# Kernel tuning notes

Hardware: AMD Instinct MI355X
Metric: run time of the kernel (lower is better)

## Reference

```python
import jax, jax.numpy as jnp
import numpy as np

N_NODES = 10000
N_EDGES = 640000
HID = 128


def setup_inputs() -> dict:
    key = jax.random.key(0)
    ks = jax.random.split(key, 8)
    h = jax.random.normal(ks[0], (N_NODES, HID), dtype=jnp.float32)
    edge_index = jax.random.randint(ks[1], (2, N_EDGES), 0, N_NODES, dtype=jnp.int64)
    edge_attr = jax.random.normal(ks[2], (N_EDGES, 1), dtype=jnp.float32)
    s1 = 1.0 / np.sqrt(2 * HID + 1)
    s2 = 1.0 / np.sqrt(HID)
    s3 = 1.0 / np.sqrt(2 * HID)
    return {
        "h": h,
        "edge_index": edge_index,
        "edge_attr": edge_attr,
        "msg_w1": jax.random.normal(ks[3], (2 * HID + 1, HID), dtype=jnp.float32) * s1,
        "msg_b1": jnp.zeros((HID,), dtype=jnp.float32),
        "msg_w2": jax.random.normal(ks[4], (HID, HID), dtype=jnp.float32) * s2,
        "msg_b2": jnp.zeros((HID,), dtype=jnp.float32),
        "upd_w1": jax.random.normal(ks[5], (2 * HID, HID), dtype=jnp.float32) * s3,
        "upd_b1": jnp.zeros((HID,), dtype=jnp.float32),
        "upd_w2": jax.random.normal(ks[6], (HID, HID), dtype=jnp.float32) * s2,
        "upd_b2": jnp.zeros((HID,), dtype=jnp.float32),
    }


def reference(h, edge_index, edge_attr, msg_w1, msg_b1, msg_w2, msg_b2,
              upd_w1, upd_b1, upd_w2, upd_b2):
    src, dst = edge_index[0], edge_index[1]
    # gather -> concat: [E, 2*HID+1]
    m_in = jnp.concatenate([h[src], h[dst], edge_attr], axis=1)
    # message MLP
    msg = jax.nn.relu(m_in @ msg_w1 + msg_b1) @ msg_w2 + msg_b2
    # scatter-add over destination nodes: [N, HID]
    agg = jax.ops.segment_sum(msg, dst, num_segments=h.shape[0])
    # update MLP with residual
    upd_in = jnp.concatenate([h, agg], axis=1)
    upd = jax.nn.relu(upd_in @ upd_w1 + upd_b1) @ upd_w2 + upd_b2
    return h + upd
```

## Files before the change

kernel.cpp:

```cpp
#include <hip/hip_runtime.h>
#include <hip/hip_bf16.h>

#define HID 128
#define NNODES 10000
#define NEDGES 640000
#define NBIN 625
#define NPB 16
#define BINCAP 1408
#define SCATB 250
#define EPT 10
#define SLAB 2560
#define PBOS 640

typedef __attribute__((ext_vector_type(8))) short bf16x8;
typedef __attribute__((ext_vector_type(4))) float f32x4;

__device__ inline short f2bf(float f) {
  unsigned u = __builtin_bit_cast(unsigned, f);
  u = (u + 0x7fffu + ((u >> 16) & 1u)) >> 16;
  return (short)u;
}
__device__ inline float bf2f(unsigned short u) {
  unsigned ui = ((unsigned)u) << 16;
  return __builtin_bit_cast(float, ui);
}

__global__ __launch_bounds__(256) void k_partA(
    const int* __restrict__ eidxraw, const float* __restrict__ ea,
    uint2* __restrict__ part, int* __restrict__ pbo,
    const float* __restrict__ h,
    const float* __restrict__ mw1, const float* __restrict__ mw2,
    const float* __restrict__ uw1, const float* __restrict__ uw2,
    short* __restrict__ pW2, short* __restrict__ pU1, short* __restrict__ pU2,
    const float* __restrict__ b1,
    short* __restrict__ Xs, short* __restrict__ cvecbf) {
  __shared__ int histL[NBIN + 1];
  __shared__ int offsL[NBIN + 1];
  __shared__ int spL[256];
  __shared__ __align__(16) uint2 slab[SLAB];
  const int bid = blockIdx.x;
  const int tid = threadIdx.x;

  if (bid < SCATB) {
    for (int i = tid; i < NBIN + 1; i += 256) histL[i] = 0;
    __syncthreads();
    bool is64 = true;
#pragma unroll
    for (int k = 0; k < 16; ++k) is64 = is64 && (eidxraw[2 * k + 1] == 0);
    unsigned pk[EPT];
    float av[EPT];
    const int ebase = bid * SLAB;
#pragma unroll
    for (int r = 0; r < EPT; ++r) {
      int e = ebase + r * 256 + tid;
      int sv = is64 ? eidxraw[2 * e] : eidxraw[e];
      int dv = is64 ? eidxraw[2 * (NEDGES + e)] : eidxraw[NEDGES + e];
      pk[r] = ((unsigned)dv << 16) | (unsigned)sv;
      av[r] = ea[e];
      atomicAdd(&histL[dv >> 4], 1);
    }
    __syncthreads();
    int c0 = 0, c1 = 0, c2 = 0;
    {
      int b0 = tid * 3;
      if (b0 < NBIN) c0 = histL[b0];
      if (b0 + 1 < NBIN) c1 = histL[b0 + 1];
      if (b0 + 2 < NBIN) c2 = histL[b0 + 2];
    }
    int s = c0 + c1 + c2;
    spL[tid] = s;
    __syncthreads();
    for (int d = 1; d < 256; d <<= 1) {
      int v = (tid >= d) ? spL[tid - d] : 0;
      __syncthreads();
      spL[tid] += v;
      __syncthreads();
    }
    int run = spL[tid] - s;
    {
      int b0 = tid * 3;
      if (b0 < NBIN)     { offsL[b0] = run;     histL[b0] = run;     run += c0; }
      if (b0 + 1 < NBIN) { offsL[b0 + 1] = run; histL[b0 + 1] = run; run += c1; }
      if (b0 + 2 < NBIN) { offsL[b0 + 2] = run; histL[b0 + 2] = run; }
    }
    if (tid == 255) offsL[NBIN] = spL[255];
    __syncthreads();
#pragma unroll
    for (int r = 0; r < EPT; ++r) {
      int bin = pk[r] >> 20;
      int pos = atomicAdd(&histL[bin], 1);
      slab[pos] = make_uint2(pk[r], __builtin_bit_cast(unsigned, av[r]));
    }
    __syncthreads();
    for (int i = tid; i < SLAB; i += 256) part[bid * SLAB + i] = slab[i];
    for (int i = tid; i < NBIN + 1; i += 256) pbo[bid * PBOS + i] = offsL[i];
  } else if (bid < 282) {
    int pb = bid - SCATB;
    const float* W; short* outp; int t;
    if (pb < 8)       { W = mw2; outp = pW2; t = pb * 256; }
    else if (pb < 24) { W = uw1; outp = pU1; t = (pb - 8) * 256; }
    else              { W = uw2; outp = pU2; t = (pb - 24) * 256; }
    t += tid;
    int ll = t & 63, nt = (t >> 6) & 7, kt = t >> 9;
    int col = nt * 16 + (ll & 15);
    int k0 = kt * 32 + ((ll >> 4) << 3);
    bf16x8 o;
#pragma unroll
    for (int j = 0; j < 8; ++j) o[j] = f2bf(W[(k0 + j) * HID + col]);
    reinterpret_cast<bf16x8*>(outp)[t] = o;
  } else {
    const int wv = tid >> 6, l = tid & 63;
    const int lr = l & 15, lg = l >> 4;
    const int rbase = (bid - 282) * 64 + wv * 16;
    int rA = rbase + lr;
    if (rA > NNODES - 1) rA = NNODES - 1;
    const float* hrow = h + (size_t)rA * HID;
    const float* W1a = mw1;
    const float* W1b = mw1 + 128 * HID;

    const f32x4 zero = {0.f, 0.f, 0.f, 0.f};
    f32x4 accA[8], accB[8];
#pragma unroll
    for (int nt = 0; nt < 8; ++nt) { accA[nt] = zero; accB[nt] = zero; }
#pragma unroll
    for (int kt = 0; kt < 4; ++kt) {
      f32x4 a0 = *reinterpret_cast<const f32x4*>(hrow + kt * 32 + lg * 8);
      f32x4 a1 = *reinterpret_cast<const f32x4*>(hrow + kt * 32 + lg * 8 + 4);
      bf16x8 af;
#pragma unroll
      for (int j = 0; j < 4; ++j) { af[j] = f2bf(a0[j]); af[4 + j] = f2bf(a1[j]); }
      const int k0 = kt * 32 + lg * 8;
#pragma unroll
      for (int nt = 0; nt < 8; ++nt) {
        const int col = nt * 16 + lr;
        bf16x8 bfa, bfb;
#pragma unroll
        for (int j = 0; j < 8; ++j) {
          bfa[j] = f2bf(W1a[(k0 + j) * HID + col]);
          bfb[j] = f2bf(W1b[(k0 + j) * HID + col]);
        }
        accA[nt] = __builtin_amdgcn_mfma_f32_16x16x32_bf16(af, bfa, accA[nt], 0, 0, 0);
        accB[nt] = __builtin_amdgcn_mfma_f32_16x16x32_bf16(af, bfb, accB[nt], 0, 0, 0);
      }
    }
#pragma unroll
    for (int nt = 0; nt < 8; ++nt) {
      const int col = nt * 16 + lr;
      const float bb = b1[col];
#pragma unroll
      for (int i = 0; i < 4; ++i) {
        int row = rbase + lg * 4 + i;
        if (row < NNODES) {
          ((unsigned short*)Xs)[row * HID + col] = (unsigned short)f2bf(accA[nt][i]);
          ((unsigned short*)cvecbf)[row * HID + col] = (unsigned short)f2bf(accB[nt][i] + bb);
        }
      }
    }
  }
}

__global__ __launch_bounds__(256) void k_merged(
    const short* __restrict__ Xs, const uint2* __restrict__ part,
    const int* __restrict__ pbo, const short* __restrict__ cvecbf,
    const float* __restrict__ w1raw, const float* __restrict__ hf,
    const short* __restrict__ pW2, const float* __restrict__ b2,
    const short* __restrict__ pU1, const float* __restrict__ bu1,
    const short* __restrict__ pU2, const float* __restrict__ bu2,
    float* __restrict__ out) {
  __shared__ __align__(16) uint2 eraw[BINCAP];
  __shared__ __align__(16) uint2 efin[BINCAP];
  __shared__ __align__(16) short ldsR[NPB][136];
  __shared__ int spL[256];
  __shared__ int cnt16[NPB], off16[NPB], cur16[NPB];
  short* ldsA = (short*)eraw;
  short* ldsB = (short*)efin;
  const int b = blockIdx.x;
  const int tid = threadIdx.x;
  const int wv = tid >> 6, l = tid & 63;
  const int lr = l & 15, lg = l >> 4;
  const int nb = b * NPB;

  if (tid < NPB) cnt16[tid] = 0;
  int o0 = 0, cnt_t = 0;
  if (tid < SCATB) {
    o0 = pbo[tid * PBOS + b];
    cnt_t = pbo[tid * PBOS + b + 1] - o0;
  }
  spL[tid] = cnt_t;
  __syncthreads();
  for (int d = 1; d < 256; d <<= 1) {
    int v = (tid >= d) ? spL[tid - d] : 0;
    __syncthreads();
    spL[tid] += v;
    __syncthreads();
  }
  const int base = spL[tid] - cnt_t;
  for (int i = 0; i < cnt_t; ++i) {
    uint2 ent = part[tid * SLAB + o0 + i];
    int pos = base + i;
    if (pos < BINCAP) {
      atomicAdd(&cnt16[(int)(ent.x >> 16) & 15], 1);
      eraw[pos] = ent;
    }
  }
  __syncthreads();
  int total = spL[255];
  if (total > BINCAP) total = BINCAP;
  if (tid < NPB) {
    int v = cnt16[tid];
    int x = v;
#pragma unroll
    for (int d = 1; d < NPB; d <<= 1) {
      int y = __shfl_up(x, d);
      if (tid >= d) x += y;
    }
    off16[tid] = x - v;
    cur16[tid] = x - v;
  }
  __syncthreads();
  for (int i = tid; i < total; i += 256) {
    uint2 ent = eraw[i];
    int local = (int)(ent.x >> 16) & 15;
    int pos = atomicAdd(&cur16[local], 1);
    efin[pos] = make_uint2(ent.x & 0xFFFFu, ent.y);
  }
  __syncthreads();

  float wl[8];
  {
    f32x4 w0 = *reinterpret_cast<const f32x4*>(w1raw + 256 * HID + lr * 8);
    f32x4 w1v = *reinterpret_cast<const f32x4*>(w1raw + 256 * HID + lr * 8 + 4);
#pragma unroll
    for (int k = 0; k < 4; ++k) { wl[k] = w0[k]; wl[k + 4] = w1v[k]; }
  }

#pragma unroll
  for (int q = 0; q < 4; ++q) {
    const int local = wv * 4 + q;
    const int node = nb + local;
    const int off = off16[local];
    const int deg = cnt16[local];
    float cv[8];
    {
      bf16x8 cvv = *reinterpret_cast<const bf16x8*>(cvecbf + node * HID + lr * 8);
#pragma unroll
      for (int k = 0; k < 8; ++k) cv[k] = bf2f((unsigned short)cvv[k]);
    }
    float acc[8];
#pragma unroll
    for (int k = 0; k < 8; ++k) acc[k] = 0.f;

    const int deg16 = deg & ~15;
    for (int j0 = 0; j0 < deg16; j0 += 16) {
      bf16x8 xs_[4];
      float av_[4];
#pragma unroll
      for (int u = 0; u < 4; ++u) {
        uint2 ent = efin[off + j0 + u * 4 + lg];
        av_[u] = __builtin_bit_cast(float, ent.y);
        xs_[u] = *reinterpret_cast<const bf16x8*>(Xs + (int)ent.x * HID + lr * 8);
      }
#pragma unroll
      for (int u = 0; u < 4; ++u)
#pragma unroll
        for (int k = 0; k < 8; ++k)
          acc[k] += fmaxf(fmaf(av_[u], wl[k], bf2f((unsigned short)xs_[u][k]) + cv[k]), 0.f);
    }
    if (deg16 < deg) {
      bf16x8 xs_[4];
      float av_[4];
      bool val_[4];
#pragma unroll
      for (int u = 0; u < 4; ++u) {
        int j = deg16 + u * 4 + lg;
        val_[u] = (j < deg);
        int jc = val_[u] ? j : (deg > 0 ? deg - 1 : 0);
        uint2 ent = efin[off + jc];
        av_[u] = __builtin_bit_cast(float, ent.y);
        xs_[u] = *reinterpret_cast<const bf16x8*>(Xs + (int)ent.x * HID + lr * 8);
      }
#pragma unroll
      for (int u = 0; u < 4; ++u)
#pragma unroll
        for (int k = 0; k < 8; ++k) {
          float v = fmaxf(fmaf(av_[u], wl[k], bf2f((unsigned short)xs_[u][k]) + cv[k]), 0.f);
          acc[k] += val_[u] ? v : 0.f;
        }
    }
#pragma unroll
    for (int k = 0; k < 8; ++k) {
      acc[k] += __shfl_xor(acc[k], 16);
      acc[k] += __shfl_xor(acc[k], 32);
    }
    if (l < 16) {
      bf16x8 r;
#pragma unroll
      for (int k = 0; k < 8; ++k) r[k] = f2bf(acc[k]);
      *reinterpret_cast<bf16x8*>(&ldsR[local][lr * 8]) = r;
    }
  }
  __syncthreads();

  const int nt0 = wv * 2;
  const f32x4 zero = {0.f, 0.f, 0.f, 0.f};

  f32x4 acc0[2] = {zero, zero};
#pragma unroll
  for (int kt = 0; kt < 4; ++kt) {
    bf16x8 af = *reinterpret_cast<const bf16x8*>(&ldsR[lr][kt * 32 + lg * 8]);
#pragma unroll
    for (int t = 0; t < 2; ++t) {
      bf16x8 bf = reinterpret_cast<const bf16x8*>(pW2)[(kt * 8 + nt0 + t) * 64 + l];
      acc0[t] = __builtin_amdgcn_mfma_f32_16x16x32_bf16(af, bf, acc0[t], 0, 0, 0);
    }
  }
#pragma unroll
  for (int t = 0; t < 2; ++t) {
    const int col = (nt0 + t) * 16 + lr;
    const float bb = b2[col];
#pragma unroll
    for (int i = 0; i < 4; ++i) {
      int row = lg * 4 + i;
      float degr = (float)cnt16[row];
      ldsA[row * 136 + col] = f2bf(acc0[t][i] + degr * bb);
    }
  }
  __syncthreads();

  f32x4 acc1[2] = {zero, zero};
  const float* hrow = hf + (size_t)(nb + lr) * HID;
#pragma unroll
  for (int kt = 0; kt < 8; ++kt) {
    bf16x8 af;
    if (kt < 4) {
      f32x4 a0 = *reinterpret_cast<const f32x4*>(hrow + kt * 32 + lg * 8);
      f32x4 a1 = *reinterpret_cast<const f32x4*>(hrow + kt * 32 + lg * 8 + 4);
#pragma unroll
      for (int j = 0; j < 4; ++j) { af[j] = f2bf(a0[j]); af[4 + j] = f2bf(a1[j]); }
    } else {
      af = *reinterpret_cast<const bf16x8*>(&ldsA[lr * 136 + (kt - 4) * 32 + lg * 8]);
    }
#pragma unroll
    for (int t = 0; t < 2; ++t) {
      bf16x8 bf = reinterpret_cast<const bf16x8*>(pU1)[(kt * 8 + nt0 + t) * 64 + l];
      acc1[t] = __builtin_amdgcn_mfma_f32_16x16x32_bf16(af, bf, acc1[t], 0, 0, 0);
    }
  }
#pragma unroll
  for (int t = 0; t < 2; ++t) {
    const int col = (nt0 + t) * 16 + lr;
    const float bb = bu1[col];
#pragma unroll
    for (int i = 0; i < 4; ++i)
      ldsB[(lg * 4 + i) * 136 + col] = f2bf(fmaxf(acc1[t][i] + bb, 0.f));
  }
  __syncthreads();

  f32x4 acc2[2] = {zero, zero};
#pragma unroll
  for (int kt = 0; kt < 4; ++kt) {
    bf16x8 af = *reinterpret_cast<const bf16x8*>(&ldsB[lr * 136 + kt * 32 + lg * 8]);
#pragma unroll
    for (int t = 0; t < 2; ++t) {
      bf16x8 bf = reinterpret_cast<const bf16x8*>(pU2)[(kt * 8 + nt0 + t) * 64 + l];
      acc2[t] = __builtin_amdgcn_mfma_f32_16x16x32_bf16(af, bf, acc2[t], 0, 0, 0);
    }
  }
#pragma unroll
  for (int t = 0; t < 2; ++t) {
    const int col = (nt0 + t) * 16 + lr;
    const float bb = bu2[col];
#pragma unroll
    for (int i = 0; i < 4; ++i) {
      int row = nb + lg * 4 + i;
      out[row * HID + col] = hf[row * HID + col] + acc2[t][i] + bb;
    }
  }
}

extern "C" void kernel_launch(void* const* d_in, const int* in_sizes, int n_in,
                              void* d_out, int out_size, void* d_ws, size_t ws_size,
                              hipStream_t stream) {
  const float* h    = (const float*)d_in[0];
  const int*   eidx = (const int*)d_in[1];
  const float* ea   = (const float*)d_in[2];
  const float* mw1  = (const float*)d_in[3];
  const float* mb1  = (const float*)d_in[4];
  const float* mw2  = (const float*)d_in[5];
  const float* mb2  = (const float*)d_in[6];
  const float* uw1  = (const float*)d_in[7];
  const float* ub1  = (const float*)d_in[8];
  const float* uw2  = (const float*)d_in[9];
  const float* ub2  = (const float*)d_in[10];
  float* out = (float*)d_out;

  char* ws = (char*)d_ws;
  uint2* part   = (uint2*)(ws + 0);
  int*   pbo    = (int*)(ws + 5120000);
  short* Xs     = (short*)(ws + 5760000);
  short* cvecbf = (short*)(ws + 8320000);
  short* pW2    = (short*)(ws + 10880000);
  short* pU1    = (short*)(ws + 10912768);
  short* pU2    = (short*)(ws + 10978304);

  k_partA<<<439, 256, 0, stream>>>(eidx, ea, part, pbo, h, mw1, mw2, uw1, uw2,
                                   pW2, pU1, pU2, mb1, Xs, cvecbf);
  k_merged<<<NBIN, 256, 0, stream>>>(Xs, part, pbo, cvecbf, mw1, h,
                                     pW2, mb2, pU1, ub1, pU2, ub2, out);
}
```

Before: 61.71 us.

## Switch edge message stage to packed fp16 math and transpose partition offsets

Node projections Xs and cvec are now stored as fp16 and produced with f16 MFMA instead of bf16. The per-edge relu-accumulate loop runs in packed half2 arithmetic with fp16 accumulators, which halves the VALU instruction count and removes the bf16-to-float conversions. The partition offset table is transposed so the merged kernel's per-thread reads of pboT are coalesced. Accumulating sums in fp16 over high-degree nodes risks precision loss or overflow.

```diff
diff --git a/kernel.cpp b/kernel.cpp
--- a/kernel.cpp
+++ b/kernel.cpp
@@ -10,9 +10,11 @@
 #define SCATB 250
 #define EPT 10
 #define SLAB 2560
-#define PBOS 640
+#define PBOT_S 256
 
 typedef __attribute__((ext_vector_type(8))) short bf16x8;
+typedef __attribute__((ext_vector_type(8))) _Float16 h8;
+typedef __attribute__((ext_vector_type(2))) _Float16 h2;
 typedef __attribute__((ext_vector_type(4))) float f32x4;
 
 __device__ inline short f2bf(float f) {
@@ -20,20 +22,16 @@
   u = (u + 0x7fffu + ((u >> 16) & 1u)) >> 16;
   return (short)u;
 }
-__device__ inline float bf2f(unsigned short u) {
-  unsigned ui = ((unsigned)u) << 16;
-  return __builtin_bit_cast(float, ui);
-}
 
 __global__ __launch_bounds__(256) void k_partA(
     const int* __restrict__ eidxraw, const float* __restrict__ ea,
-    uint2* __restrict__ part, int* __restrict__ pbo,
+    uint2* __restrict__ part, int* __restrict__ pboT,
     const float* __restrict__ h,
     const float* __restrict__ mw1, const float* __restrict__ mw2,
     const float* __restrict__ uw1, const float* __restrict__ uw2,
     short* __restrict__ pW2, short* __restrict__ pU1, short* __restrict__ pU2,
     const float* __restrict__ b1,
-    short* __restrict__ Xs, short* __restrict__ cvecbf) {
+    _Float16* __restrict__ Xs, _Float16* __restrict__ cvecH) {
   __shared__ int histL[NBIN + 1];
   __shared__ int offsL[NBIN + 1];
   __shared__ int spL[256];
@@ -93,7 +91,7 @@
     }
     __syncthreads();
     for (int i = tid; i < SLAB; i += 256) part[bid * SLAB + i] = slab[i];
-    for (int i = tid; i < NBIN + 1; i += 256) pbo[bid * PBOS + i] = offsL[i];
+    for (int i = tid; i < NBIN + 1; i += 256) pboT[i * PBOT_S + bid] = offsL[i];
   } else if (bid < 282) {
     int pb = bid - SCATB;
     const float* W; short* outp; int t;
@@ -126,21 +124,21 @@
     for (int kt = 0; kt < 4; ++kt) {
       f32x4 a0 = *reinterpret_cast<const f32x4*>(hrow + kt * 32 + lg * 8);
       f32x4 a1 = *reinterpret_cast<const f32x4*>(hrow + kt * 32 + lg * 8 + 4);
-      bf16x8 af;
-#pragma unroll
-      for (int j = 0; j < 4; ++j) { af[j] = f2bf(a0[j]); af[4 + j] = f2bf(a1[j]); }
+      h8 af;
+#pragma unroll
+      for (int j = 0; j < 4; ++j) { af[j] = (_Float16)a0[j]; af[4 + j] = (_Float16)a1[j]; }
       const int k0 = kt * 32 + lg * 8;
 #pragma unroll
       for (int nt = 0; nt < 8; ++nt) {
         const int col = nt * 16 + lr;
-        bf16x8 bfa, bfb;
+        h8 bfa, bfb;
 #pragma unroll
         for (int j = 0; j < 8; ++j) {
-          bfa[j] = f2bf(W1a[(k0 + j) * HID + col]);
-          bfb[j] = f2bf(W1b[(k0 + j) * HID + col]);
+          bfa[j] = (_Float16)W1a[(k0 + j) * HID + col];
+          bfb[j] = (_Float16)W1b[(k0 + j) * HID + col];
         }
-        accA[nt] = __builtin_amdgcn_mfma_f32_16x16x32_bf16(af, bfa, accA[nt], 0, 0, 0);
-        accB[nt] = __builtin_amdgcn_mfma_f32_16x16x32_bf16(af, bfb, accB[nt], 0, 0, 0);
+        accA[nt] = __builtin_amdgcn_mfma_f32_16x16x32_f16(af, bfa, accA[nt], 0, 0, 0);
+        accB[nt] = __builtin_amdgcn_mfma_f32_16x16x32_f16(af, bfb, accB[nt], 0, 0, 0);
       }
     }
 #pragma unroll
@@ -151,8 +149,8 @@
       for (int i = 0; i < 4; ++i) {
         int row = rbase + lg * 4 + i;
         if (row < NNODES) {
-          ((unsigned short*)Xs)[row * HID + col] = (unsigned short)f2bf(accA[nt][i]);
-          ((unsigned short*)cvecbf)[row * HID + col] = (unsigned short)f2bf(accB[nt][i] + bb);
+          Xs[row * HID + col] = (_Float16)accA[nt][i];
+          cvecH[row * HID + col] = (_Float16)(accB[nt][i] + bb);
         }
       }
     }
@@ -160,8 +158,8 @@
 }
 
 __global__ __launch_bounds__(256) void k_merged(
-    const short* __restrict__ Xs, const uint2* __restrict__ part,
-    const int* __restrict__ pbo, const short* __restrict__ cvecbf,
+    const _Float16* __restrict__ Xs, const uint2* __restrict__ part,
+    const int* __restrict__ pboT, const _Float16* __restrict__ cvecH,
     const float* __restrict__ w1raw, const float* __restrict__ hf,
     const short* __restrict__ pW2, const float* __restrict__ b2,
     const short* __restrict__ pU1, const float* __restrict__ bu1,
@@ -183,8 +181,8 @@
   if (tid < NPB) cnt16[tid] = 0;
   int o0 = 0, cnt_t = 0;
   if (tid < SCATB) {
-    o0 = pbo[tid * PBOS + b];
-    cnt_t = pbo[tid * PBOS + b + 1] - o0;
+    o0 = pboT[b * PBOT_S + tid];
+    cnt_t = pboT[(b + 1) * PBOT_S + tid] - o0;
   }
   spL[tid] = cnt_t;
   __syncthreads();
@@ -226,13 +224,16 @@
   }
   __syncthreads();
 
-  float wl[8];
+  h2 wl2[4];
   {
     f32x4 w0 = *reinterpret_cast<const f32x4*>(w1raw + 256 * HID + lr * 8);
     f32x4 w1v = *reinterpret_cast<const f32x4*>(w1raw + 256 * HID + lr * 8 + 4);
-#pragma unroll
-    for (int k = 0; k < 4; ++k) { wl[k] = w0[k]; wl[k + 4] = w1v[k]; }
-  }
+    wl2[0] = h2{(_Float16)w0[0], (_Float16)w0[1]};
+    wl2[1] = h2{(_Float16)w0[2], (_Float16)w0[3]};
+    wl2[2] = h2{(_Float16)w1v[0], (_Float16)w1v[1]};
+    wl2[3] = h2{(_Float16)w1v[2], (_Float16)w1v[3]};
+  }
+  const h2 zero2 = h2{(_Float16)0.f, (_Float16)0.f};
 
 #pragma unroll
   for (int q = 0; q < 4; ++q) {
@@ -240,35 +241,38 @@
     const int node = nb + local;
     const int off = off16[local];
     const int deg = cnt16[local];
-    float cv[8];
+    h2 cv2[4];
     {
-      bf16x8 cvv = *reinterpret_cast<const bf16x8*>(cvecbf + node * HID + lr * 8);
-#pragma unroll
-      for (int k = 0; k < 8; ++k) cv[k] = bf2f((unsigned short)cvv[k]);
-    }
-    float acc[8];
-#pragma unroll
-    for (int k = 0; k < 8; ++k) acc[k] = 0.f;
+      h8 c = *reinterpret_cast<const h8*>(cvecH + node * HID + lr * 8);
+#pragma unroll
+      for (int p = 0; p < 4; ++p) cv2[p] = h2{c[2 * p], c[2 * p + 1]};
+    }
+    h2 s2[4] = {zero2, zero2, zero2, zero2};
 
     const int deg16 = deg & ~15;
     for (int j0 = 0; j0 < deg16; j0 += 16) {
-      bf16x8 xs_[4];
-      float av_[4];
+      h8 xs_[4];
+      h2 av2_[4];
 #pragma unroll
       for (int u = 0; u < 4; ++u) {
         uint2 ent = efin[off + j0 + u * 4 + lg];
-        av_[u] = __builtin_bit_cast(float, ent.y);
-        xs_[u] = *reinterpret_cast<const bf16x8*>(Xs + (int)ent.x * HID + lr * 8);
-      }
-#pragma unroll
-      for (int u = 0; u < 4; ++u)
-#pragma unroll
-        for (int k = 0; k < 8; ++k)
-          acc[k] += fmaxf(fmaf(av_[u], wl[k], bf2f((unsigned short)xs_[u][k]) + cv[k]), 0.f);
+        _Float16 a = (_Float16)__builtin_bit_cast(float, ent.y);
+        av2_[u] = h2{a, a};
+        xs_[u] = *reinterpret_cast<const h8*>(Xs + (int)ent.x * HID + lr * 8);
+      }
+#pragma unroll
+      for (int u = 0; u < 4; ++u) {
+#pragma unroll
+        for (int p = 0; p < 4; ++p) {
+          h2 x2 = h2{xs_[u][2 * p], xs_[u][2 * p + 1]};
+          h2 t = x2 + cv2[p] + av2_[u] * wl2[p];
+          s2[p] += __builtin_elementwise_max(t, zero2);
+        }
+      }
     }
     if (deg16 < deg) {
-      bf16x8 xs_[4];
-      float av_[4];
+      h8 xs_[4];
+      h2 av2_[4];
       bool val_[4];
 #pragma unroll
       for (int u = 0; u < 4; ++u) {
@@ -276,16 +280,26 @@
         val_[u] = (j < deg);
         int jc = val_[u] ? j : (deg > 0 ? deg - 1 : 0);
         uint2 ent = efin[off + jc];
-        av_[u] = __builtin_bit_cast(float, ent.y);
-        xs_[u] = *reinterpret_cast<const bf16x8*>(Xs + (int)ent.x * HID + lr * 8);
-      }
-#pragma unroll
-      for (int u = 0; u < 4; ++u)
-#pragma unroll
-        for (int k = 0; k < 8; ++k) {
-          float v = fmaxf(fmaf(av_[u], wl[k], bf2f((unsigned short)xs_[u][k]) + cv[k]), 0.f);
-          acc[k] += val_[u] ? v : 0.f;
+        _Float16 a = (_Float16)__builtin_bit_cast(float, ent.y);
+        av2_[u] = h2{a, a};
+        xs_[u] = *reinterpret_cast<const h8*>(Xs + (int)ent.x * HID + lr * 8);
+      }
+#pragma unroll
+      for (int u = 0; u < 4; ++u) {
+#pragma unroll
+        for (int p = 0; p < 4; ++p) {
+          h2 x2 = h2{xs_[u][2 * p], xs_[u][2 * p + 1]};
+          h2 t = x2 + cv2[p] + av2_[u] * wl2[p];
+          t = __builtin_elementwise_max(t, zero2);
+          s2[p] += val_[u] ? t : zero2;
         }
+      }
+    }
+    float acc[8];
+#pragma unroll
+    for (int p = 0; p < 4; ++p) {
+      acc[2 * p] = (float)s2[p][0];
+      acc[2 * p + 1] = (float)s2[p][1];
     }
 #pragma unroll
     for (int k = 0; k < 8; ++k) {
@@ -395,16 +409,16 @@
   float* out = (float*)d_out;
 
   char* ws = (char*)d_ws;
-  uint2* part   = (uint2*)(ws + 0);
-  int*   pbo    = (int*)(ws + 5120000);
-  short* Xs     = (short*)(ws + 5760000);
-  short* cvecbf = (short*)(ws + 8320000);
-  short* pW2    = (short*)(ws + 10880000);
-  short* pU1    = (short*)(ws + 10912768);
-  short* pU2    = (short*)(ws + 10978304);
-
-  k_partA<<<439, 256, 0, stream>>>(eidx, ea, part, pbo, h, mw1, mw2, uw1, uw2,
-                                   pW2, pU1, pU2, mb1, Xs, cvecbf);
-  k_merged<<<NBIN, 256, 0, stream>>>(Xs, part, pbo, cvecbf, mw1, h,
+  uint2*     part  = (uint2*)(ws + 0);
+  int*       pboT  = (int*)(ws + 5120000);
+  _Float16*  Xs    = (_Float16*)(ws + 5761024);
+  _Float16*  cvecH = (_Float16*)(ws + 8321024);
+  short*     pW2   = (short*)(ws + 10881024);
+  short*     pU1   = (short*)(ws + 10913792);
+  short*     pU2   = (short*)(ws + 10979328);
+
+  k_partA<<<439, 256, 0, stream>>>(eidx, ea, part, pboT, h, mw1, mw2, uw1, uw2,
+                                   pW2, pU1, pU2, mb1, Xs, cvecH);
+  k_merged<<<NBIN, 256, 0, stream>>>(Xs, part, pboT, cvecH, mw1, h,
                                      pW2, mb2, pU1, ub1, pU2, ub2, out);
 }
```

New measurement: 58.73 us. 1.05x faster.
